# Kernel optimization log

Hardware: AMD Instinct MI355X
Metric: run time of the kernel (lower is better)

The kernel has to match this reference:

```python
import jax, jax.numpy as jnp
import numpy as np

B, N, C, H = 4, 4096, 1024, 16
HD = C // H  # head_dim = 64
EPS = 1e-6


def setup_inputs() -> dict:
    key = jax.random.key(0)
    ks = jax.random.split(key, 5)
    x = jax.random.normal(ks[0], (B, N, C), dtype=jnp.float32)
    s_in = 1.0 / np.sqrt(C)
    W_qkv = jax.random.normal(ks[1], (C, 3 * C), dtype=jnp.float32) * s_in
    b_qkv = jnp.zeros((3 * C,), dtype=jnp.float32)
    W_out = jax.random.normal(ks[2], (C, C), dtype=jnp.float32) * s_in
    b_out = jnp.zeros((C,), dtype=jnp.float32)
    return {"x": x, "W_qkv": W_qkv, "b_qkv": b_qkv, "W_out": W_out, "b_out": b_out}


def reference(x, W_qkv, b_qkv, W_out, b_out):
    # qkv projection: (B, N, 3C)
    qkv = jnp.einsum('bnc,cf->bnf', x, W_qkv) + b_qkv
    # rearrange 'b n (h d) -> b h n d' with d = 3*head_dim, then chunk into q,k,v
    qkv = qkv.reshape(B, N, H, 3 * HD).transpose(0, 2, 1, 3)  # (B,H,N,3*HD)
    q, k, v = jnp.split(qkv, 3, axis=-1)  # each (B,H,N,HD)
    # silu feature map
    q = jax.nn.silu(q)
    k = jax.nn.silu(k)
    # linear attention: state = k^T @ v per head  -> (B,H,HD,HD)
    state = jnp.einsum('bhnd,bhne->bhde', k, v)
    k_sum = k.sum(axis=2)  # (B,H,HD)
    num = jnp.einsum('bhnd,bhde->bhne', q, state)  # (B,H,N,HD)
    den = jnp.einsum('bhnd,bhd->bhn', q, k_sum)[..., None]  # (B,H,N,1)
    out = num / (den + EPS)
    # 'b h n d -> b n (h d)'
    out = out.transpose(0, 2, 1, 3).reshape(B, N, C)
    return jnp.einsum('bnc,cf->bnf', out, W_out) + b_out
```

## Files before the change

### kernel.cpp

```cpp
#include <hip/hip_runtime.h>

typedef unsigned short u16;
typedef unsigned int u32;
typedef __attribute__((ext_vector_type(8))) short short8;
typedef __attribute__((ext_vector_type(8))) _Float16 half8;
typedef __attribute__((ext_vector_type(4))) float f32x4;

#define DEV __device__ __forceinline__

DEV void async_copy16(const void* g, void* l) {
  __builtin_amdgcn_global_load_lds((const __attribute__((address_space(1))) u32*)g,
                                   (__attribute__((address_space(3))) u32*)l, 16, 0, 0);
}
DEV float bf2f(u16 u) { return __uint_as_float(((u32)u) << 16); }
DEV u16 f2bf(float f) {
  u32 x = __float_as_uint(f);
  return (u16)((x + 0x7fffu + ((x >> 16) & 1u)) >> 16);
}
DEV u16 f2h_bits(float f) { _Float16 h = (_Float16)f; return __builtin_bit_cast(u16, h); }
DEV float h2f_bits(u16 b) { return (float)__builtin_bit_cast(_Float16, b); }
DEV float silu_f(float x) { return x / (1.0f + __expf(-x)); }

DEV void stage_tile(const u16* __restrict__ G, size_t grow_base, int k0, u16* L, int t) {
#pragma unroll
  for (int it = 0; it < 2; ++it) {
    int c = t + it * 256;
    int r = c >> 2, j = c & 3;
    int js = j ^ ((r >> 1) & 3);
    async_copy16(G + ((grow_base + (size_t)r) << 10) + k0 + js * 8,
                 (char*)L + (size_t)c * 16);
  }
}
DEV half8 frag(const u16* L, int rr, int lq) {
  int sw = lq ^ ((rr >> 1) & 3);
  return *(const half8*)((const char*)L + (size_t)rr * 64 + sw * 16);
}
DEV short8 frag_s(const u16* L, int rr, int lq) {
  int sw = lq ^ ((rr >> 1) & 3);
  return *(const short8*)((const char*)L + (size_t)rr * 64 + sw * 16);
}

__global__ __launch_bounds__(256) void transpose_k(const float* __restrict__ W,
                                                   u16* __restrict__ Wt,
                                                   int K, int N) {
  __shared__ float s[32][33];
  int t = threadIdx.x;
  int tx = t & 31, ty = t >> 5;
  int ntk = K >> 5;
  int bk = blockIdx.x % ntk, bn = blockIdx.x / ntk;
  int k0 = bk * 32, n0 = bn * 32;
#pragma unroll
  for (int i = 0; i < 4; ++i)
    s[ty + 8 * i][tx] = W[(size_t)(k0 + ty + 8 * i) * N + n0 + tx];
  __syncthreads();
#pragma unroll
  for (int i = 0; i < 4; ++i) {
    int r = ty + 8 * i;
    Wt[(size_t)(n0 + r) * K + k0 + tx] = f2bf(s[tx][r]);
  }
}

__global__ __launch_bounds__(256) void split_x(const float* __restrict__ x,
                                               u16* __restrict__ X0,
                                               u16* __restrict__ X1) {
  int i = (blockIdx.x * 256 + threadIdx.x) * 4;
  float4 v = *(const float4*)&x[i];
  ushort4 h0, h1;
  h0.x = f2h_bits(v.x); h1.x = f2h_bits((v.x - h2f_bits(h0.x)) * 4096.0f);
  h0.y = f2h_bits(v.y); h1.y = f2h_bits((v.y - h2f_bits(h0.y)) * 4096.0f);
  h0.z = f2h_bits(v.z); h1.z = f2h_bits((v.z - h2f_bits(h0.z)) * 4096.0f);
  h0.w = f2h_bits(v.w); h1.w = f2h_bits((v.w - h2f_bits(h0.w)) * 4096.0f);
  *(ushort4*)&X0[i] = h0;
  *(ushort4*)&X1[i] = h1;
}

__global__ __launch_bounds__(256) void split_w(const float* __restrict__ W,
                                               u16* __restrict__ W0t,
                                               u16* __restrict__ W1t) {
  __shared__ float s[32][33];
  int t = threadIdx.x;
  int tx = t & 31, ty = t >> 5;
  int bk = blockIdx.x & 31, bn = blockIdx.x >> 5;
  int k0 = bk * 32, n0 = bn * 32;
#pragma unroll
  for (int i = 0; i < 4; ++i)
    s[ty + 8 * i][tx] = W[(size_t)(k0 + ty + 8 * i) * 3072 + n0 + tx];
  __syncthreads();
#pragma unroll
  for (int i = 0; i < 4; ++i) {
    int r = ty + 8 * i;
    int col = n0 + r;
    int h = col / 192, rem = col - h * 192;
    int cty = rem >> 6, d = rem & 63;
    int pcol = cty * 1024 + h * 64 + d;
    float v = s[tx][r];
    u16 h0 = f2h_bits(v);
    u16 h1 = f2h_bits((v - h2f_bits(h0)) * 4096.0f);
    size_t o = (size_t)pcol * 1024 + k0 + tx;
    W0t[o] = h0;
    W1t[o] = h1;
  }
}

__global__ __launch_bounds__(256, 2) void gemm_qk_f16(
    const u16* __restrict__ X0, const u16* __restrict__ X1,
    const u16* __restrict__ W0, const u16* __restrict__ W1,
    const float* __restrict__ bq,
    float* __restrict__ Qf, float* __restrict__ Kf) {
  __shared__ u16 lA0[128 * 32];
  __shared__ u16 lA1[128 * 32];
  __shared__ u16 lB0[128 * 32];
  __shared__ u16 lB1[128 * 32];
  int t = threadIdx.x;
  int w = t >> 6, l = t & 63;
  int wr = w >> 1, wc = w & 1;
  int lr = l & 15, lq = l >> 4;
  int mb = blockIdx.y * 128, nb = blockIdx.x * 128;
  int cty = nb >> 10;
  f32x4 aM[4][4] = {};
  f32x4 aC[4][4] = {};

  for (int k0 = 0; k0 < 1024; k0 += 32) {
#pragma unroll
    for (int it = 0; it < 2; ++it) {
      int c = t + it * 256;
      int r = c >> 2, j = c & 3;
      int js = j ^ ((r >> 1) & 3);
      size_t goA = (((size_t)(mb + r)) << 10) + k0 + js * 8;
      size_t goB = (((size_t)(nb + r)) << 10) + k0 + js * 8;
      async_copy16(X0 + goA, (char*)lA0 + (size_t)c * 16);
      async_copy16(X1 + goA, (char*)lA1 + (size_t)c * 16);
      async_copy16(W0 + goB, (char*)lB0 + (size_t)c * 16);
      async_copy16(W1 + goB, (char*)lB1 + (size_t)c * 16);
    }
    __syncthreads();
    half8 b0[4], b1[4];
#pragma unroll
    for (int nn = 0; nn < 4; ++nn) {
      int rr = wc * 64 + nn * 16 + lr;
      b0[nn] = frag(lB0, rr, lq);
      b1[nn] = frag(lB1, rr, lq);
    }
#pragma unroll
    for (int m = 0; m < 4; ++m) {
      int rr = wr * 64 + m * 16 + lr;
      half8 a0 = frag(lA0, rr, lq);
      half8 a1 = frag(lA1, rr, lq);
#pragma unroll
      for (int nn = 0; nn < 4; ++nn) {
        aM[m][nn] = __builtin_amdgcn_mfma_f32_16x16x32_f16(a0, b0[nn], aM[m][nn], 0, 0, 0);
        aC[m][nn] = __builtin_amdgcn_mfma_f32_16x16x32_f16(a0, b1[nn], aC[m][nn], 0, 0, 0);
        aC[m][nn] = __builtin_amdgcn_mfma_f32_16x16x32_f16(a1, b0[nn], aC[m][nn], 0, 0, 0);
      }
    }
    __syncthreads();
  }

  const float cscale = 2.44140625e-4f;
  float* dst = (cty == 0) ? Qf : Kf;
#pragma unroll
  for (int nn = 0; nn < 4; ++nn) {
    int col = nb + wc * 64 + nn * 16 + lr;
    int h = (col & 1023) >> 6, d0 = col & 63;
    float bias = bq[h * 192 + cty * 64 + d0];
#pragma unroll
    for (int m = 0; m < 4; ++m)
#pragma unroll
      for (int j = 0; j < 4; ++j) {
        int row = mb + wr * 64 + m * 16 + lq * 4 + j;
        int b = row >> 12, n = row & 4095;
        size_t base = (((size_t)(b * 16 + h) * 4096 + n) << 6) + d0;
        float val = aM[m][nn][j] + aC[m][nn][j] * cscale + bias;
        dst[base] = silu_f(val);
      }
  }
}

__global__ __launch_bounds__(256) void gemm_v_f16(
    const u16* __restrict__ X0, const u16* __restrict__ W0,
    const float* __restrict__ bq, u16* __restrict__ Vb) {
  __shared__ u16 lA0[128 * 32];
  __shared__ u16 lB0[128 * 32];
  int t = threadIdx.x;
  int w = t >> 6, l = t & 63;
  int wr = w >> 1, wc = w & 1;
  int lr = l & 15, lq = l >> 4;
  int mb = blockIdx.y * 128, nb = 2048 + blockIdx.x * 128;
  f32x4 aM[4][4] = {};

  for (int k0 = 0; k0 < 1024; k0 += 32) {
    stage_tile(X0, mb, k0, lA0, t);
    stage_tile(W0, nb, k0, lB0, t);
    __syncthreads();
    half8 b0[4];
#pragma unroll
    for (int nn = 0; nn < 4; ++nn) b0[nn] = frag(lB0, wc * 64 + nn * 16 + lr, lq);
#pragma unroll
    for (int m = 0; m < 4; ++m) {
      half8 a0 = frag(lA0, wr * 64 + m * 16 + lr, lq);
#pragma unroll
      for (int nn = 0; nn < 4; ++nn)
        aM[m][nn] = __builtin_amdgcn_mfma_f32_16x16x32_f16(a0, b0[nn], aM[m][nn], 0, 0, 0);
    }
    __syncthreads();
  }
#pragma unroll
  for (int nn = 0; nn < 4; ++nn) {
    int col = nb + wc * 64 + nn * 16 + lr;
    int h = (col & 1023) >> 6, d0 = col & 63;
    float bias = bq[h * 192 + 128 + d0];
#pragma unroll
    for (int m = 0; m < 4; ++m)
#pragma unroll
      for (int j = 0; j < 4; ++j) {
        int row = mb + wr * 64 + m * 16 + lq * 4 + j;
        int b = row >> 12, n = row & 4095;
        size_t base = (((size_t)(b * 16 + h) * 4096 + n) << 6) + d0;
        Vb[base] = f2bf(aM[m][nn][j] + bias);
      }
  }
}

__global__ __launch_bounds__(256) void gemm_qkv(const float* __restrict__ X,
                                                const float* __restrict__ Wq,
                                                const float* __restrict__ bq,
                                                float* __restrict__ Qf,
                                                float* __restrict__ Kf,
                                                u16* __restrict__ Vb) {
  __shared__ float sA[16 * 132];
  __shared__ float sB[16 * 128];
  int t = threadIdx.x;
  int tm = t >> 4, tn = t & 15;
  int mb = blockIdx.y * 128, nb = blockIdx.x * 128;
  float acc[8][8] = {};

  for (int k0 = 0; k0 < 1024; k0 += 16) {
#pragma unroll
    for (int it = 0; it < 2; ++it) {
      int c = t + it * 256;
      int m = c >> 2, kc = (c & 3) * 4;
      float4 v = *(const float4*)&X[(size_t)(mb + m) * 1024 + k0 + kc];
      sA[(kc + 0) * 132 + m] = v.x;
      sA[(kc + 1) * 132 + m] = v.y;
      sA[(kc + 2) * 132 + m] = v.z;
      sA[(kc + 3) * 132 + m] = v.w;
      int kr = c >> 5, nc = (c & 31) * 4;
      async_copy16(&Wq[(size_t)(k0 + kr) * 3072 + nb + nc], (char*)sB + (size_t)c * 16);
    }
    __syncthreads();
#pragma unroll
    for (int k = 0; k < 16; ++k) {
      float4 a0 = *(const float4*)&sA[k * 132 + tm * 8];
      float4 a1 = *(const float4*)&sA[k * 132 + tm * 8 + 4];
      float4 b0 = *(const float4*)&sB[k * 128 + tn * 8];
      float4 b1 = *(const float4*)&sB[k * 128 + tn * 8 + 4];
      const float av[8] = {a0.x, a0.y, a0.z, a0.w, a1.x, a1.y, a1.z, a1.w};
      const float bv[8] = {b0.x, b0.y, b0.z, b0.w, b1.x, b1.y, b1.z, b1.w};
#pragma unroll
      for (int i = 0; i < 8; ++i)
#pragma unroll
        for (int j = 0; j < 8; ++j) acc[i][j] = fmaf(av[i], bv[j], acc[i][j]);
    }
    __syncthreads();
  }

  int c0 = nb + tn * 8;
  int h = c0 / 192, rem = c0 % 192;
  int ty = rem >> 6, d0 = rem & 63;
  float bb[8];
#pragma unroll
  for (int j = 0; j < 8; ++j) bb[j] = bq[c0 + j];
#pragma unroll
  for (int i = 0; i < 8; ++i) {
    int r = mb + tm * 8 + i;
    int b = r >> 12, n = r & 4095;
    size_t base = (((size_t)(b * 16 + h) * 4096 + n) << 6) + d0;
    if (ty == 2) {
      u16 pk[8];
#pragma unroll
      for (int j = 0; j < 8; ++j) pk[j] = f2bf(acc[i][j] + bb[j]);
      *(short8*)&Vb[base] = *(short8*)pk;
    } else {
      float* dst = (ty == 0) ? Qf : Kf;
#pragma unroll
      for (int j = 0; j < 8; ++j) dst[base + j] = silu_f(acc[i][j] + bb[j]);
    }
  }
}

__global__ __launch_bounds__(256) void state_partial(const float* __restrict__ Kf,
                                                     const u16* __restrict__ Vb,
                                                     float* __restrict__ stateP,
                                                     float* __restrict__ ksumP) {
  int bh = blockIdx.y, ch = blockIdx.x, t = threadIdx.x;
  __shared__ float sK[64 * 64];
  __shared__ u16 sV[64 * 64];
  __shared__ float sred[256];
  int n0 = ch * 512;
  size_t base = ((size_t)bh * 4096 + n0) << 6;
  float acc[4][4] = {};
  int te = t & 15, td = t >> 4;
  int kd = t & 63, kq = t >> 6;
  float kacc = 0.0f;

  for (int sc = 0; sc < 8; ++sc) {
    const float* gk = Kf + base + (size_t)sc * 64 * 64;
    const u16* gv = Vb + base + (size_t)sc * 64 * 64;
#pragma unroll
    for (int it = 0; it < 4; ++it)
      async_copy16(gk + (size_t)(t + it * 256) * 4, (char*)sK + (size_t)(t + it * 256) * 16);
#pragma unroll
    for (int it = 0; it < 2; ++it)
      async_copy16(gv + (size_t)(t + it * 256) * 8, (char*)sV + (size_t)(t + it * 256) * 16);
    __syncthreads();
#pragma unroll 4
    for (int n = 0; n < 64; ++n) {
      float4 k4 = *(const float4*)&sK[n * 64 + td * 4];
      const float ka[4] = {k4.x, k4.y, k4.z, k4.w};
      ushort4 vv = *(const ushort4*)&sV[n * 64 + te * 4];
      const float va[4] = {bf2f(vv.x), bf2f(vv.y), bf2f(vv.z), bf2f(vv.w)};
#pragma unroll
      for (int i = 0; i < 4; ++i)
#pragma unroll
        for (int j = 0; j < 4; ++j) acc[i][j] = fmaf(ka[i], va[j], acc[i][j]);
    }
#pragma unroll
    for (int i = 0; i < 16; ++i) kacc += sK[(kq * 16 + i) * 64 + kd];
    __syncthreads();
  }
  size_t pb = ((size_t)bh * 8 + ch) * 4096;
#pragma unroll
  for (int i = 0; i < 4; ++i)
#pragma unroll
    for (int j = 0; j < 4; ++j)
      stateP[pb + (size_t)(td * 4 + i) * 64 + te * 4 + j] = acc[i][j];

  sred[t] = kacc;
  __syncthreads();
  if (t < 64)
    ksumP[((size_t)bh * 8 + ch) * 64 + t] = sred[t] + sred[t + 64] + sred[t + 128] + sred[t + 192];
}

__global__ __launch_bounds__(256) void attn_out(const float* __restrict__ Qf,
                                                const float* __restrict__ stateP,
                                                const float* __restrict__ ksumP,
                                                u16* __restrict__ outb) {
  int bh = blockIdx.y, chnk = blockIdx.x, t = threadIdx.x;
  __shared__ float sS[4096];
  __shared__ float sk[64];
#pragma unroll
  for (int i = 0; i < 16; ++i) {
    int e = t + i * 256;
    float s = 0.0f;
#pragma unroll
    for (int c = 0; c < 8; ++c) s += stateP[((size_t)bh * 8 + c) * 4096 + e];
    sS[e] = s;
  }
  if (t < 64) {
    float s = 0.0f;
#pragma unroll
    for (int c = 0; c < 8; ++c) s += ksumP[((size_t)bh * 8 + c) * 64 + t];
    sk[t] = s;
  }
  __syncthreads();

  int n = chnk * 256 + t;
  size_t qb = ((size_t)bh * 4096 + n) << 6;
  float4 a4[16] = {};
  float den = 0.0f;
#pragma unroll 4
  for (int dd = 0; dd < 16; ++dd) {
    float4 q4 = *(const float4*)&Qf[qb + dd * 4];
    const float qa[4] = {q4.x, q4.y, q4.z, q4.w};
#pragma unroll
    for (int jj = 0; jj < 4; ++jj) {
      int d = dd * 4 + jj;
      float qf = qa[jj];
      den = fmaf(qf, sk[d], den);
      const float4* srow = (const float4*)&sS[d * 64];
#pragma unroll
      for (int e4 = 0; e4 < 16; ++e4) {
        float4 s = srow[e4];
        a4[e4].x = fmaf(qf, s.x, a4[e4].x);
        a4[e4].y = fmaf(qf, s.y, a4[e4].y);
        a4[e4].z = fmaf(qf, s.z, a4[e4].z);
        a4[e4].w = fmaf(qf, s.w, a4[e4].w);
      }
    }
  }
  float rden = 1.0f / (den + 1e-6f);
  int b = bh >> 4, h = bh & 15;
  size_t ob = ((size_t)(b * 4096 + n) << 10) + h * 64;
#pragma unroll
  for (int e4 = 0; e4 < 16; ++e4) {
    ushort4 u;
    u.x = f2bf(a4[e4].x * rden);
    u.y = f2bf(a4[e4].y * rden);
    u.z = f2bf(a4[e4].z * rden);
    u.w = f2bf(a4[e4].w * rden);
    *(ushort4*)&outb[ob + e4 * 4] = u;
  }
}

__global__ __launch_bounds__(256) void gemm_out(const u16* __restrict__ A,
                                                const u16* __restrict__ Bt,
                                                const float* __restrict__ bias,
                                                float* __restrict__ C) {
  __shared__ u16 lA[2][128 * 32];
  __shared__ u16 lB[2][128 * 32];
  int t = threadIdx.x;
  int w = t >> 6, l = t & 63;
  int wr = w >> 1, wc = w & 1;
  int lr = l & 15, lq = l >> 4;
  int mb = blockIdx.y * 128, nb = blockIdx.x * 128;
  f32x4 acc[4][4] = {};

  stage_tile(A, mb, 0, lA[0], t);
  stage_tile(Bt, nb, 0, lB[0], t);
  __syncthreads();
  int cur = 0;
  for (int k0 = 0; k0 < 1024; k0 += 32) {
    if (k0 + 32 < 1024) {
      stage_tile(A, mb, k0 + 32, lA[cur ^ 1], t);
      stage_tile(Bt, nb, k0 + 32, lB[cur ^ 1], t);
    }
    short8 af[4], bf[4];
#pragma unroll
    for (int m = 0; m < 4; ++m) af[m] = frag_s(lA[cur], wr * 64 + m * 16 + lr, lq);
#pragma unroll
    for (int nn = 0; nn < 4; ++nn) bf[nn] = frag_s(lB[cur], wc * 64 + nn * 16 + lr, lq);
#pragma unroll
    for (int m = 0; m < 4; ++m)
#pragma unroll
      for (int nn = 0; nn < 4; ++nn)
        acc[m][nn] = __builtin_amdgcn_mfma_f32_16x16x32_bf16(af[m], bf[nn], acc[m][nn], 0, 0, 0);
    __syncthreads();
    cur ^= 1;
  }

#pragma unroll
  for (int m = 0; m < 4; ++m)
#pragma unroll
    for (int nn = 0; nn < 4; ++nn) {
      int col = nb + wc * 64 + nn * 16 + lr;
      float bc = bias[col];
#pragma unroll
      for (int j = 0; j < 4; ++j) {
        int row = mb + wr * 64 + m * 16 + lq * 4 + j;
        C[((size_t)row << 10) + col] = acc[m][nn][j] + bc;
      }
    }
}

extern "C" void kernel_launch(void* const* d_in, const int* in_sizes, int n_in,
                              void* d_out, int out_size, void* d_ws, size_t ws_size,
                              hipStream_t stream) {
  const float* x    = (const float*)d_in[0];
  const float* Wqkv = (const float*)d_in[1];
  const float* bqkv = (const float*)d_in[2];
  const float* Wout = (const float*)d_in[3];
  const float* bout = (const float*)d_in[4];
  float* out = (float*)d_out;

  char* w = (char*)d_ws;
  const size_t offK  = 0;
  const size_t offV  = offK + 67108864ULL;
  const size_t offSP = offV + 33554432ULL;
  const size_t offKP = offSP + 8388608ULL;
  const size_t offWT = offKP + 131072ULL;
  const size_t need_base = offWT + 2097152ULL;
  const size_t offX0 = need_base;
  const size_t offX1 = offX0 + 33554432ULL;
  const size_t offW0 = offX1 + 33554432ULL;
  const size_t offW1 = offW0 + 6291456ULL;
  const size_t need_fast = offW1 + 6291456ULL;

  if (ws_size < need_base) return;

  float* Kf     = (float*)(w + offK);
  u16*   outb   = (u16*)(w + offK);
  u16*   Vb     = (u16*)(w + offV);
  float* stateP = (float*)(w + offSP);
  float* ksumP  = (float*)(w + offKP);
  u16*   WoutT  = (u16*)(w + offWT);
  float* Qf     = out;

  transpose_k<<<dim3(1024), dim3(256), 0, stream>>>(Wout, WoutT, 1024, 1024);

  if (ws_size >= need_fast) {
    u16* X0 = (u16*)(w + offX0);
    u16* X1 = (u16*)(w + offX1);
    u16* W0 = (u16*)(w + offW0);
    u16* W1 = (u16*)(w + offW1);
    split_x<<<dim3(16384), dim3(256), 0, stream>>>(x, X0, X1);
    split_w<<<dim3(3072), dim3(256), 0, stream>>>(Wqkv, W0, W1);
    gemm_qk_f16<<<dim3(16, 128), dim3(256), 0, stream>>>(X0, X1, W0, W1, bqkv, Qf, Kf);
    gemm_v_f16<<<dim3(8, 128), dim3(256), 0, stream>>>(X0, W0, bqkv, Vb);
  } else {
    gemm_qkv<<<dim3(24, 128), dim3(256), 0, stream>>>(x, Wqkv, bqkv, Qf, Kf, Vb);
  }

  state_partial<<<dim3(8, 64), dim3(256), 0, stream>>>(Kf, Vb, stateP, ksumP);
  attn_out<<<dim3(16, 64), dim3(256), 0, stream>>>(Qf, stateP, ksumP, outb);
  gemm_out<<<dim3(8, 128), dim3(256), 0, stream>>>(outb, WoutT, bout, out);
}
```

Baseline: 469.0 us.

## Merge V projection into QK GEMM, split state reduction, single-buffer output GEMM

```diff
diff --git a/kernel.cpp b/kernel.cpp
--- a/kernel.cpp
+++ b/kernel.cpp
@@ -102,11 +102,11 @@
   }
 }
 
-__global__ __launch_bounds__(256, 2) void gemm_qk_f16(
+__global__ __launch_bounds__(256, 2) void gemm_qkv_f16(
     const u16* __restrict__ X0, const u16* __restrict__ X1,
     const u16* __restrict__ W0, const u16* __restrict__ W1,
     const float* __restrict__ bq,
-    float* __restrict__ Qf, float* __restrict__ Kf) {
+    float* __restrict__ Qf, float* __restrict__ Kf, u16* __restrict__ Vb) {
   __shared__ u16 lA0[128 * 32];
   __shared__ u16 lA1[128 * 32];
   __shared__ u16 lB0[128 * 32];
@@ -117,6 +117,43 @@
   int lr = l & 15, lq = l >> 4;
   int mb = blockIdx.y * 128, nb = blockIdx.x * 128;
   int cty = nb >> 10;
+
+  if (cty == 2) {
+    f32x4 aM[4][4] = {};
+    for (int k0 = 0; k0 < 1024; k0 += 32) {
+      stage_tile(X0, mb, k0, lA0, t);
+      stage_tile(W0, nb, k0, lB0, t);
+      __syncthreads();
+      half8 b0[4];
+#pragma unroll
+      for (int nn = 0; nn < 4; ++nn) b0[nn] = frag(lB0, wc * 64 + nn * 16 + lr, lq);
+#pragma unroll
+      for (int m = 0; m < 4; ++m) {
+        half8 a0 = frag(lA0, wr * 64 + m * 16 + lr, lq);
+#pragma unroll
+        for (int nn = 0; nn < 4; ++nn)
+          aM[m][nn] = __builtin_amdgcn_mfma_f32_16x16x32_f16(a0, b0[nn], aM[m][nn], 0, 0, 0);
+      }
+      __syncthreads();
+    }
+#pragma unroll
+    for (int nn = 0; nn < 4; ++nn) {
+      int col = nb + wc * 64 + nn * 16 + lr;
+      int h = (col & 1023) >> 6, d0 = col & 63;
+      float bias = bq[h * 192 + 128 + d0];
+#pragma unroll
+      for (int m = 0; m < 4; ++m)
+#pragma unroll
+        for (int j = 0; j < 4; ++j) {
+          int row = mb + wr * 64 + m * 16 + lq * 4 + j;
+          int b = row >> 12, n = row & 4095;
+          size_t base = (((size_t)(b * 16 + h) * 4096 + n) << 6) + d0;
+          Vb[base] = f2bf(aM[m][nn][j] + bias);
+        }
+    }
+    return;
+  }
+
   f32x4 aM[4][4] = {};
   f32x4 aC[4][4] = {};
 
@@ -172,51 +209,6 @@
         size_t base = (((size_t)(b * 16 + h) * 4096 + n) << 6) + d0;
         float val = aM[m][nn][j] + aC[m][nn][j] * cscale + bias;
         dst[base] = silu_f(val);
-      }
-  }
-}
-
-__global__ __launch_bounds__(256) void gemm_v_f16(
-    const u16* __restrict__ X0, const u16* __restrict__ W0,
-    const float* __restrict__ bq, u16* __restrict__ Vb) {
-  __shared__ u16 lA0[128 * 32];
-  __shared__ u16 lB0[128 * 32];
-  int t = threadIdx.x;
-  int w = t >> 6, l = t & 63;
-  int wr = w >> 1, wc = w & 1;
-  int lr = l & 15, lq = l >> 4;
-  int mb = blockIdx.y * 128, nb = 2048 + blockIdx.x * 128;
-  f32x4 aM[4][4] = {};
-
-  for (int k0 = 0; k0 < 1024; k0 += 32) {
-    stage_tile(X0, mb, k0, lA0, t);
-    stage_tile(W0, nb, k0, lB0, t);
-    __syncthreads();
-    half8 b0[4];
-#pragma unroll
-    for (int nn = 0; nn < 4; ++nn) b0[nn] = frag(lB0, wc * 64 + nn * 16 + lr, lq);
-#pragma unroll
-    for (int m = 0; m < 4; ++m) {
-      half8 a0 = frag(lA0, wr * 64 + m * 16 + lr, lq);
-#pragma unroll
-      for (int nn = 0; nn < 4; ++nn)
-        aM[m][nn] = __builtin_amdgcn_mfma_f32_16x16x32_f16(a0, b0[nn], aM[m][nn], 0, 0, 0);
-    }
-    __syncthreads();
-  }
-#pragma unroll
-  for (int nn = 0; nn < 4; ++nn) {
-    int col = nb + wc * 64 + nn * 16 + lr;
-    int h = (col & 1023) >> 6, d0 = col & 63;
-    float bias = bq[h * 192 + 128 + d0];
-#pragma unroll
-    for (int m = 0; m < 4; ++m)
-#pragma unroll
-      for (int j = 0; j < 4; ++j) {
-        int row = mb + wr * 64 + m * 16 + lq * 4 + j;
-        int b = row >> 12, n = row & 4095;
-        size_t base = (((size_t)(b * 16 + h) * 4096 + n) << 6) + d0;
-        Vb[base] = f2bf(aM[m][nn][j] + bias);
       }
   }
 }
@@ -341,9 +333,30 @@
     ksumP[((size_t)bh * 8 + ch) * 64 + t] = sred[t] + sred[t + 64] + sred[t + 128] + sred[t + 192];
 }
 
+__global__ __launch_bounds__(256) void reduce_state(const float* __restrict__ stateP,
+                                                    const float* __restrict__ ksumP,
+                                                    float* __restrict__ stateF,
+                                                    float* __restrict__ ksumF) {
+  int bh = blockIdx.x, t = threadIdx.x;
+#pragma unroll
+  for (int i = 0; i < 16; ++i) {
+    int e = t + i * 256;
+    float s = 0.0f;
+#pragma unroll
+    for (int c = 0; c < 8; ++c) s += stateP[((size_t)bh * 8 + c) * 4096 + e];
+    stateF[(size_t)bh * 4096 + e] = s;
+  }
+  if (t < 64) {
+    float s = 0.0f;
+#pragma unroll
+    for (int c = 0; c < 8; ++c) s += ksumP[((size_t)bh * 8 + c) * 64 + t];
+    ksumF[(size_t)bh * 64 + t] = s;
+  }
+}
+
 __global__ __launch_bounds__(256) void attn_out(const float* __restrict__ Qf,
-                                                const float* __restrict__ stateP,
-                                                const float* __restrict__ ksumP,
+                                                const float* __restrict__ stateF,
+                                                const float* __restrict__ ksumF,
                                                 u16* __restrict__ outb) {
   int bh = blockIdx.y, chnk = blockIdx.x, t = threadIdx.x;
   __shared__ float sS[4096];
@@ -351,17 +364,9 @@
 #pragma unroll
   for (int i = 0; i < 16; ++i) {
     int e = t + i * 256;
-    float s = 0.0f;
-#pragma unroll
-    for (int c = 0; c < 8; ++c) s += stateP[((size_t)bh * 8 + c) * 4096 + e];
-    sS[e] = s;
-  }
-  if (t < 64) {
-    float s = 0.0f;
-#pragma unroll
-    for (int c = 0; c < 8; ++c) s += ksumP[((size_t)bh * 8 + c) * 64 + t];
-    sk[t] = s;
-  }
+    sS[e] = stateF[(size_t)bh * 4096 + e];
+  }
+  if (t < 64) sk[t] = ksumF[(size_t)bh * 64 + t];
   __syncthreads();
 
   int n = chnk * 256 + t;
@@ -406,8 +411,8 @@
                                                 const u16* __restrict__ Bt,
                                                 const float* __restrict__ bias,
                                                 float* __restrict__ C) {
-  __shared__ u16 lA[2][128 * 32];
-  __shared__ u16 lB[2][128 * 32];
+  __shared__ u16 lA[128 * 32];
+  __shared__ u16 lB[128 * 32];
   int t = threadIdx.x;
   int w = t >> 6, l = t & 63;
   int wr = w >> 1, wc = w & 1;
@@ -415,27 +420,21 @@
   int mb = blockIdx.y * 128, nb = blockIdx.x * 128;
   f32x4 acc[4][4] = {};
 
-  stage_tile(A, mb, 0, lA[0], t);
-  stage_tile(Bt, nb, 0, lB[0], t);
-  __syncthreads();
-  int cur = 0;
   for (int k0 = 0; k0 < 1024; k0 += 32) {
-    if (k0 + 32 < 1024) {
-      stage_tile(A, mb, k0 + 32, lA[cur ^ 1], t);
-      stage_tile(Bt, nb, k0 + 32, lB[cur ^ 1], t);
-    }
+    stage_tile(A, mb, k0, lA, t);
+    stage_tile(Bt, nb, k0, lB, t);
+    __syncthreads();
     short8 af[4], bf[4];
 #pragma unroll
-    for (int m = 0; m < 4; ++m) af[m] = frag_s(lA[cur], wr * 64 + m * 16 + lr, lq);
-#pragma unroll
-    for (int nn = 0; nn < 4; ++nn) bf[nn] = frag_s(lB[cur], wc * 64 + nn * 16 + lr, lq);
+    for (int m = 0; m < 4; ++m) af[m] = frag_s(lA, wr * 64 + m * 16 + lr, lq);
+#pragma unroll
+    for (int nn = 0; nn < 4; ++nn) bf[nn] = frag_s(lB, wc * 64 + nn * 16 + lr, lq);
 #pragma unroll
     for (int m = 0; m < 4; ++m)
 #pragma unroll
       for (int nn = 0; nn < 4; ++nn)
         acc[m][nn] = __builtin_amdgcn_mfma_f32_16x16x32_bf16(af[m], bf[nn], acc[m][nn], 0, 0, 0);
     __syncthreads();
-    cur ^= 1;
   }
 
 #pragma unroll
@@ -468,7 +467,9 @@
   const size_t offSP = offV + 33554432ULL;
   const size_t offKP = offSP + 8388608ULL;
   const size_t offWT = offKP + 131072ULL;
-  const size_t need_base = offWT + 2097152ULL;
+  const size_t offSF = offWT + 2097152ULL;
+  const size_t offKF = offSF + 1048576ULL;
+  const size_t need_base = offKF + 16384ULL;
   const size_t offX0 = need_base;
   const size_t offX1 = offX0 + 33554432ULL;
   const size_t offW0 = offX1 + 33554432ULL;
@@ -483,6 +484,8 @@
   float* stateP = (float*)(w + offSP);
   float* ksumP  = (float*)(w + offKP);
   u16*   WoutT  = (u16*)(w + offWT);
+  float* stateF = (float*)(w + offSF);
+  float* ksumF  = (float*)(w + offKF);
   float* Qf     = out;
 
   transpose_k<<<dim3(1024), dim3(256), 0, stream>>>(Wout, WoutT, 1024, 1024);
@@ -494,13 +497,13 @@
     u16* W1 = (u16*)(w + offW1);
     split_x<<<dim3(16384), dim3(256), 0, stream>>>(x, X0, X1);
     split_w<<<dim3(3072), dim3(256), 0, stream>>>(Wqkv, W0, W1);
-    gemm_qk_f16<<<dim3(16, 128), dim3(256), 0, stream>>>(X0, X1, W0, W1, bqkv, Qf, Kf);
-    gemm_v_f16<<<dim3(8, 128), dim3(256), 0, stream>>>(X0, W0, bqkv, Vb);
+    gemm_qkv_f16<<<dim3(24, 128), dim3(256), 0, stream>>>(X0, X1, W0, W1, bqkv, Qf, Kf, Vb);
   } else {
     gemm_qkv<<<dim3(24, 128), dim3(256), 0, stream>>>(x, Wqkv, bqkv, Qf, Kf, Vb);
   }
 
   state_partial<<<dim3(8, 64), dim3(256), 0, stream>>>(Kf, Vb, stateP, ksumP);
-  attn_out<<<dim3(16, 64), dim3(256), 0, stream>>>(Qf, stateP, ksumP, outb);
+  reduce_state<<<dim3(64), dim3(256), 0, stream>>>(stateP, ksumP, stateF, ksumF);
+  attn_out<<<dim3(16, 64), dim3(256), 0, stream>>>(Qf, stateF, ksumF, outb);
   gemm_out<<<dim3(8, 128), dim3(256), 0, stream>>>(outb, WoutT, bout, out);
 }
```

After: 461.5 us. Within noise of the previous version (-1.6%).
